# Optimization experiments

Measured on AMD Instinct MI355X. Metric: run time of the kernel, lower is better.

## Reference

```python
import jax, jax.numpy as jnp
import numpy as np

N_NODES = 100000
D = 256
N_EDGES = 500000
N_CLASSES = 4


def setup_inputs() -> dict:
    key = jax.random.key(0)
    k1, k2, k3, k4 = jax.random.split(key, 4)
    inp = jax.random.normal(k1, (N_NODES, D), dtype=jnp.float32)
    r_indices = jax.random.randint(k2, (N_EDGES,), 0, N_NODES, dtype=jnp.int64)
    c_indices = jax.random.randint(k3, (N_EDGES,), 0, N_NODES, dtype=jnp.int64)
    # xavier-uniform-like init for the skinny classifier weight
    limit = float(np.sqrt(6.0 / (D + N_CLASSES)))
    weight = jax.random.uniform(k4, (D, N_CLASSES), dtype=jnp.float32,
                                minval=-limit, maxval=limit)
    return {"input": inp, "r_indices": r_indices, "c_indices": c_indices,
            "weight": weight}


def reference(input, r_indices, c_indices, weight):
    # dropout p=0.0 -> identity. Gather edge endpoints, abs diff, skinny matmul.
    diff = jnp.abs(input[r_indices] - input[c_indices])  # [E, D]
    out = jnp.einsum('ed,dc->ec', diff, weight)          # [E, C]
    return out
```

## Files before the change

kernel.cpp:

```cpp
#include <hip/hip_runtime.h>


#define NODES   100000
#define DIM     256
#define EDGES   500000
#define NCLS    4

__device__ __forceinline__ unsigned short f2bf_rne(float f) {
    union { float f; unsigned int u; } x; x.f = f;
    unsigned int r = x.u + 0x7FFFu + ((x.u >> 16) & 1u);
    return (unsigned short)(r >> 16);
}
__device__ __forceinline__ float bf_lo(unsigned int u) {
    return __uint_as_float(u << 16);
}
__device__ __forceinline__ float bf_hi(unsigned int u) {
    return __uint_as_float(u & 0xFFFF0000u);
}

__global__ __launch_bounds__(256) void cvt_bf16_kernel(
    const float* __restrict__ in,
    unsigned short* __restrict__ tbl)
{
    const int total4 = NODES * DIM / 4;
    const int stride = gridDim.x * blockDim.x;
    for (int i = blockIdx.x * blockDim.x + threadIdx.x; i < total4; i += stride) {
        const float4 v = ((const float4*)in)[i];
        ushort4 o;
        o.x = f2bf_rne(v.x);
        o.y = f2bf_rne(v.y);
        o.z = f2bf_rne(v.z);
        o.w = f2bf_rne(v.w);
        ((ushort4*)tbl)[i] = o;
    }
}

__global__ __launch_bounds__(256, 4) void edge_mlp_bf16_kernel(
    const unsigned short* __restrict__ tbl,
    const int*   __restrict__ r_idx,
    const int*   __restrict__ c_idx,
    const float* __restrict__ weight,
    float*       __restrict__ out)
{
    const int lane = threadIdx.x & 63;
    const int half = lane >> 5;
    const int hl   = lane & 31;
    const int wid  = (blockIdx.x * blockDim.x + threadIdx.x) >> 6;
    const int n_waves = (gridDim.x * blockDim.x) >> 6;

    const int d0 = hl * 8;
    float4 w[8];
    #pragma unroll
    for (int j = 0; j < 8; ++j)
        w[j] = *(const float4*)(weight + (d0 + j) * NCLS);

    for (int e = wid * 2; e < EDGES; e += n_waves * 2) {
        const int ee = e + half;
        const int r = r_idx[ee];
        const int c = c_idx[ee];

        const uint4 ua = *(const uint4*)(tbl + (size_t)r * DIM + d0);
        const uint4 ub = *(const uint4*)(tbl + (size_t)c * DIM + d0);

        float t[8];
        t[0] = fabsf(bf_lo(ua.x) - bf_lo(ub.x));
        t[1] = fabsf(bf_hi(ua.x) - bf_hi(ub.x));
        t[2] = fabsf(bf_lo(ua.y) - bf_lo(ub.y));
        t[3] = fabsf(bf_hi(ua.y) - bf_hi(ub.y));
        t[4] = fabsf(bf_lo(ua.z) - bf_lo(ub.z));
        t[5] = fabsf(bf_hi(ua.z) - bf_hi(ub.z));
        t[6] = fabsf(bf_lo(ua.w) - bf_lo(ub.w));
        t[7] = fabsf(bf_hi(ua.w) - bf_hi(ub.w));

        float4 acc = make_float4(0.f, 0.f, 0.f, 0.f);
        #pragma unroll
        for (int j = 0; j < 8; ++j) {
            acc.x += t[j] * w[j].x;
            acc.y += t[j] * w[j].y;
            acc.z += t[j] * w[j].z;
            acc.w += t[j] * w[j].w;
        }

        #pragma unroll
        for (int m = 16; m >= 1; m >>= 1) {
            acc.x += __shfl_xor(acc.x, m, 64);
            acc.y += __shfl_xor(acc.y, m, 64);
            acc.z += __shfl_xor(acc.z, m, 64);
            acc.w += __shfl_xor(acc.w, m, 64);
        }

        if (hl == 0) {
            *(float4*)(out + (size_t)ee * NCLS) = acc;
        }
    }
}

__global__ __launch_bounds__(256, 8) void edge_mlp_f32_kernel(
    const float* __restrict__ input,
    const int*   __restrict__ r_idx,
    const int*   __restrict__ c_idx,
    const float* __restrict__ weight,
    float*       __restrict__ out)
{
    const int lane = threadIdx.x & 63;
    const int wid  = (blockIdx.x * blockDim.x + threadIdx.x) >> 6;
    const int n_waves = (gridDim.x * blockDim.x) >> 6;

    const int d0 = lane * 4;
    const float4 w0 = *(const float4*)(weight + (d0 + 0) * NCLS);
    const float4 w1 = *(const float4*)(weight + (d0 + 1) * NCLS);
    const float4 w2 = *(const float4*)(weight + (d0 + 2) * NCLS);
    const float4 w3 = *(const float4*)(weight + (d0 + 3) * NCLS);

    for (int e = wid; e < EDGES; e += n_waves) {
        const int r = r_idx[e];
        const int c = c_idx[e];
        const float4 a = *(const float4*)(input + (size_t)r * DIM + d0);
        const float4 b = *(const float4*)(input + (size_t)c * DIM + d0);

        const float t0 = fabsf(a.x - b.x);
        const float t1 = fabsf(a.y - b.y);
        const float t2 = fabsf(a.z - b.z);
        const float t3 = fabsf(a.w - b.w);

        float4 acc;
        acc.x = t0 * w0.x + t1 * w1.x + t2 * w2.x + t3 * w3.x;
        acc.y = t0 * w0.y + t1 * w1.y + t2 * w2.y + t3 * w3.y;
        acc.z = t0 * w0.z + t1 * w1.z + t2 * w2.z + t3 * w3.z;
        acc.w = t0 * w0.w + t1 * w1.w + t2 * w2.w + t3 * w3.w;

        #pragma unroll
        for (int m = 32; m >= 1; m >>= 1) {
            acc.x += __shfl_xor(acc.x, m, 64);
            acc.y += __shfl_xor(acc.y, m, 64);
            acc.z += __shfl_xor(acc.z, m, 64);
            acc.w += __shfl_xor(acc.w, m, 64);
        }
        if (lane == 0) *(float4*)(out + (size_t)e * NCLS) = acc;
    }
}

extern "C" void kernel_launch(void* const* d_in, const int* in_sizes, int n_in,
                              void* d_out, int out_size, void* d_ws, size_t ws_size,
                              hipStream_t stream) {
    const float* input  = (const float*)d_in[0];
    const int*   r_idx  = (const int*)d_in[1];
    const int*   c_idx  = (const int*)d_in[2];
    const float* weight = (const float*)d_in[3];
    float* out = (float*)d_out;

    const size_t tbl_bytes = (size_t)NODES * DIM * 2;

    if (ws_size >= tbl_bytes) {
        unsigned short* tbl = (unsigned short*)d_ws;
        cvt_bf16_kernel<<<2048, 256, 0, stream>>>(input, tbl);
        edge_mlp_bf16_kernel<<<2048, 256, 0, stream>>>(tbl, r_idx, c_idx, weight, out);
    } else {
        edge_mlp_f32_kernel<<<2048, 256, 0, stream>>>(input, r_idx, c_idx, weight, out);
    }
}
```

Measured before the change: 109.4 us.

## Quantize node table to per-row int8 with scales instead of bf16

Replaces the bf16 staging table with an 8-bit offset-quantized table plus one float scale per node row, computed by a wave-per-row absmax reduction. The edge kernel gathers 8 bytes per lane per endpoint instead of 16 and dequantizes with fused multiply-adds before the abs-diff and skinny matmul. This halves gather and conversion-write traffic, at the cost of much coarser precision (about 7 bits per value), which may exceed the accuracy tolerance. It also adds an extra scale load per endpoint.

```diff
diff --git a/kernel.cpp b/kernel.cpp
--- a/kernel.cpp
+++ b/kernel.cpp
@@ -6,37 +6,38 @@
 #define EDGES   500000
 #define NCLS    4
 
-__device__ __forceinline__ unsigned short f2bf_rne(float f) {
-    union { float f; unsigned int u; } x; x.f = f;
-    unsigned int r = x.u + 0x7FFFu + ((x.u >> 16) & 1u);
-    return (unsigned short)(r >> 16);
-}
-__device__ __forceinline__ float bf_lo(unsigned int u) {
-    return __uint_as_float(u << 16);
-}
-__device__ __forceinline__ float bf_hi(unsigned int u) {
-    return __uint_as_float(u & 0xFFFF0000u);
-}
+__global__ __launch_bounds__(256) void quant_kernel(
+    const float* __restrict__ in,
+    unsigned char* __restrict__ tbl,
+    float* __restrict__ scales)
+{
+    const int lane = threadIdx.x & 63;
+    const int wid  = (blockIdx.x * blockDim.x + threadIdx.x) >> 6;
+    const int n_waves = (gridDim.x * blockDim.x) >> 6;
 
-__global__ __launch_bounds__(256) void cvt_bf16_kernel(
-    const float* __restrict__ in,
-    unsigned short* __restrict__ tbl)
-{
-    const int total4 = NODES * DIM / 4;
-    const int stride = gridDim.x * blockDim.x;
-    for (int i = blockIdx.x * blockDim.x + threadIdx.x; i < total4; i += stride) {
-        const float4 v = ((const float4*)in)[i];
-        ushort4 o;
-        o.x = f2bf_rne(v.x);
-        o.y = f2bf_rne(v.y);
-        o.z = f2bf_rne(v.z);
-        o.w = f2bf_rne(v.w);
-        ((ushort4*)tbl)[i] = o;
+    for (int row = wid; row < NODES; row += n_waves) {
+        const float4 v = *(const float4*)(in + (size_t)row * DIM + lane * 4);
+        float m = fmaxf(fmaxf(fabsf(v.x), fabsf(v.y)),
+                        fmaxf(fabsf(v.z), fabsf(v.w)));
+        #pragma unroll
+        for (int s = 32; s >= 1; s >>= 1)
+            m = fmaxf(m, __shfl_xor(m, s, 64));
+
+        const float rs = (m > 0.f) ? 127.f / m : 0.f;
+        uchar4 q;
+        q.x = (unsigned char)__float2int_rn(fmaf(v.x, rs, 128.f));
+        q.y = (unsigned char)__float2int_rn(fmaf(v.y, rs, 128.f));
+        q.z = (unsigned char)__float2int_rn(fmaf(v.z, rs, 128.f));
+        q.w = (unsigned char)__float2int_rn(fmaf(v.w, rs, 128.f));
+        *(uchar4*)(tbl + (size_t)row * DIM + lane * 4) = q;
+
+        if (lane == 0) scales[row] = (m > 0.f) ? m / 127.f : 0.f;
     }
 }
 
-__global__ __launch_bounds__(256, 4) void edge_mlp_bf16_kernel(
-    const unsigned short* __restrict__ tbl,
+__global__ __launch_bounds__(256, 4) void edge_mlp_i8_kernel(
+    const unsigned char* __restrict__ tbl,
+    const float* __restrict__ scales,
     const int*   __restrict__ r_idx,
     const int*   __restrict__ c_idx,
     const float* __restrict__ weight,
@@ -58,28 +59,35 @@
         const int ee = e + half;
         const int r = r_idx[ee];
         const int c = c_idx[ee];
+        const float sr = scales[r];
+        const float sc = scales[c];
+        const float nsc = -sc;
+        const float B = 128.f * (sc - sr);
 
-        const uint4 ua = *(const uint4*)(tbl + (size_t)r * DIM + d0);
-        const uint4 ub = *(const uint4*)(tbl + (size_t)c * DIM + d0);
-
-        float t[8];
-        t[0] = fabsf(bf_lo(ua.x) - bf_lo(ub.x));
-        t[1] = fabsf(bf_hi(ua.x) - bf_hi(ub.x));
-        t[2] = fabsf(bf_lo(ua.y) - bf_lo(ub.y));
-        t[3] = fabsf(bf_hi(ua.y) - bf_hi(ub.y));
-        t[4] = fabsf(bf_lo(ua.z) - bf_lo(ub.z));
-        t[5] = fabsf(bf_hi(ua.z) - bf_hi(ub.z));
-        t[6] = fabsf(bf_lo(ua.w) - bf_lo(ub.w));
-        t[7] = fabsf(bf_hi(ua.w) - bf_hi(ub.w));
+        const uint2 ua = *(const uint2*)(tbl + (size_t)r * DIM + d0);
+        const uint2 ub = *(const uint2*)(tbl + (size_t)c * DIM + d0);
 
         float4 acc = make_float4(0.f, 0.f, 0.f, 0.f);
-        #pragma unroll
-        for (int j = 0; j < 8; ++j) {
-            acc.x += t[j] * w[j].x;
-            acc.y += t[j] * w[j].y;
-            acc.z += t[j] * w[j].z;
-            acc.w += t[j] * w[j].w;
-        }
+        float u, t;
+
+        #define TERM(UA, UB, SH, W)                                         \
+            u = fmaf((float)((UA >> SH) & 0xffu), sr,                        \
+                     fmaf((float)((UB >> SH) & 0xffu), nsc, B));             \
+            t = fabsf(u);                                                    \
+            acc.x = fmaf(t, W.x, acc.x);                                     \
+            acc.y = fmaf(t, W.y, acc.y);                                     \
+            acc.z = fmaf(t, W.z, acc.z);                                     \
+            acc.w = fmaf(t, W.w, acc.w);
+
+        TERM(ua.x, ub.x,  0, w[0])
+        TERM(ua.x, ub.x,  8, w[1])
+        TERM(ua.x, ub.x, 16, w[2])
+        TERM(ua.x, ub.x, 24, w[3])
+        TERM(ua.y, ub.y,  0, w[4])
+        TERM(ua.y, ub.y,  8, w[5])
+        TERM(ua.y, ub.y, 16, w[6])
+        TERM(ua.y, ub.y, 24, w[7])
+        #undef TERM
 
         #pragma unroll
         for (int m = 16; m >= 1; m >>= 1) {
@@ -149,13 +157,17 @@
     const float* weight = (const float*)d_in[3];
     float* out = (float*)d_out;
 
-    const size_t tbl_bytes = (size_t)NODES * DIM * 2;
+    const size_t tbl_bytes   = (size_t)NODES * DIM;
+    const size_t scale_bytes = (size_t)NODES * sizeof(float);
 
-    if (ws_size >= tbl_bytes) {
-        unsigned short* tbl = (unsigned short*)d_ws;
-        cvt_bf16_kernel<<<2048, 256, 0, stream>>>(input, tbl);
-        edge_mlp_bf16_kernel<<<2048, 256, 0, stream>>>(tbl, r_idx, c_idx, weight, out);
+    if (ws_size >= tbl_bytes + scale_bytes) {
+        unsigned char* tbl = (unsigned char*)d_ws;
+        float* scales = (float*)((char*)d_ws + tbl_bytes);
+        quant_kernel<<<2048, 256, 0, stream>>>(input, tbl, scales);
+        edge_mlp_i8_kernel<<<2048, 256, 0, stream>>>(tbl, scales, r_idx, c_idx,
+                                                     weight, out);
     } else {
-        edge_mlp_f32_kernel<<<2048, 256, 0, stream>>>(input, r_idx, c_idx, weight, out);
+        edge_mlp_f32_kernel<<<2048, 256, 0, stream>>>(input, r_idx, c_idx,
+                                                      weight, out);
     }
 }
```

Measured after the change: 94.63 us. -13.5%, faster.
